# Kernel optimization log

Hardware: AMD Instinct MI355X
Metric: run time of the kernel (lower is better)

## Reference

```python
import jax, jax.numpy as jnp
import numpy as np

B, S, E, H, A, C = 128, 1024, 2048, 300, 5, 3


def setup_inputs() -> dict:
    key = jax.random.key(0)
    ks = jax.random.split(key, 14)
    sc = 0.05
    return {
        "h": jax.random.normal(ks[0], (B, S, H), jnp.float32),
        "edge_index": jax.random.randint(ks[1], (B, 2, E), 0, S, dtype=jnp.int32),
        "edge_weight": jax.random.uniform(ks[2], (B, E), jnp.float32),
        "aspect_pos": jax.random.randint(ks[3], (B, A), 0, S, dtype=jnp.int32),
        "W_span": jax.random.normal(ks[4], (H, H), jnp.float32) * sc,
        "b_span": jnp.zeros((H,), jnp.float32),
        "W1": jax.random.normal(ks[5], (H, H), jnp.float32) * sc,
        "b1": jnp.zeros((H,), jnp.float32),
        "W2": jax.random.normal(ks[6], (H, H), jnp.float32) * sc,
        "b2": jnp.zeros((H,), jnp.float32),
        "W_gate": jax.random.normal(ks[7], (2 * H, H), jnp.float32) * sc,
        "b_gate": jnp.zeros((H,), jnp.float32),
        "W_cls": jax.random.normal(ks[8], (H, C), jnp.float32) * sc,
        "b_cls": jnp.zeros((C,), jnp.float32),
    }


def _gcn_conv(x, src, dst, ew, W, b):
    # PyG GCNConv: xW, add self-loops (w=1), symmetric norm, scatter-sum at dst.
    n = x.shape[0]
    xw = x @ W  # [S, H]
    deg = jnp.zeros((n,), x.dtype).at[dst].add(ew) + 1.0  # +1 from self-loop
    dinv = jax.lax.rsqrt(deg)
    norm = dinv[src] * ew * dinv[dst]  # [E]
    msg = norm[:, None] * xw[src]  # [E, H]
    out = jax.ops.segment_sum(msg, dst, num_segments=n)
    out = out + xw / deg[:, None]  # self-loop: dinv[i]^2 * xw[i]
    return out + b


def reference(h, edge_index, edge_weight, aspect_pos,
              W_span, b_span, W1, b1, W2, b2, W_gate, b_gate, W_cls, b_cls):
    def per_sample(h_i, ei, ew, ap):
        # aspect-attention span pooling
        aspect_vec = h_i[ap].mean(0)  # [H]
        q = aspect_vec @ W_span + b_span
        attn = jax.nn.softmax(h_i @ q)  # [S]
        span = attn @ h_i  # [H]
        # 2-layer GCN over dependency edges
        src, dst = ei[0], ei[1]
        x = jax.nn.relu(_gcn_conv(h_i, src, dst, ew, W1, b1))
        x = _gcn_conv(x, src, dst, ew, W2, b2)
        syn = x[ap].mean(0)  # [H]
        return span, syn

    span, syn = jax.vmap(per_sample)(h, edge_index, edge_weight, aspect_pos)
    gate = jax.nn.sigmoid(jnp.concatenate([span, syn], axis=-1) @ W_gate + b_gate)
    fused = gate * syn + (1.0 - gate) * span
    return fused @ W_cls + b_cls  # [B, C]
```

## Files before the change

kernel.cpp:

```cpp
#include <hip/hip_runtime.h>
#include <math.h>

#define BB 128
#define SS 1024
#define EE 2048
#define HH 300
#define AA 5
#define CC 3
#define NB 8
#define PSTRIDE 304
#define EMAX 2049


__global__ void k_init(float* deg, float* syn) {
    int gid = blockIdx.x * blockDim.x + threadIdx.x;
    if (gid < BB * SS) deg[gid] = 1.0f;
    if (gid < BB * HH) syn[gid] = 0.0f;
}

__global__ void k_deg(const int* __restrict__ eidx, const float* __restrict__ ew,
                      float* __restrict__ deg) {
    int gid = blockIdx.x * blockDim.x + threadIdx.x;
    if (gid >= BB * EE) return;
    int b = gid >> 11;
    int e = gid & (EE - 1);
    int d = eidx[(size_t)b * 2 * EE + EE + e];
    atomicAdd(&deg[b * SS + d], ew[(size_t)b * EE + e]);
}

__global__ __launch_bounds__(320) void k_q(const float* __restrict__ h, const int* __restrict__ ap,
                                           const float* __restrict__ W_span, const float* __restrict__ b_span,
                                           float* __restrict__ qbuf) {
    int b = blockIdx.x;
    __shared__ float av[HH];
    const float* hb = h + (size_t)b * SS * HH;
    for (int j = threadIdx.x; j < HH; j += blockDim.x) {
        float s = 0.f;
        for (int a = 0; a < AA; ++a) s += hb[(size_t)ap[b * AA + a] * HH + j];
        av[j] = s * (1.0f / AA);
    }
    __syncthreads();
    for (int j = threadIdx.x; j < HH; j += blockDim.x) {
        float acc = b_span[j];
        for (int i = 0; i < HH; ++i) acc += av[i] * W_span[i * HH + j];
        qbuf[b * HH + j] = acc;
    }
}

__global__ __launch_bounds__(256) void k_span_part(const float* __restrict__ h,
                                                   const float* __restrict__ qbuf,
                                                   float* __restrict__ part) {
    int b = blockIdx.x / NB, nb = blockIdx.x % NB;
    int tid = threadIdx.x, lane = tid & 63, w = tid >> 6;
    const float* hb = h + (size_t)b * SS * HH;
    const float* qb = qbuf + b * HH;
    float qr[5];
#pragma unroll
    for (int k = 0; k < 5; ++k) { int idx = lane + 64 * k; qr[k] = (idx < HH) ? qb[idx] : 0.f; }
    float m = -INFINITY, l = 0.f;
    float acc[5] = {0.f, 0.f, 0.f, 0.f, 0.f};
    int row0 = nb * (SS / NB) + w * 32;
    for (int t = 0; t < 32; ++t) {
        const float* hr = hb + (size_t)(row0 + t) * HH;
        float hv[5]; float pd = 0.f;
#pragma unroll
        for (int k = 0; k < 5; ++k) {
            int idx = lane + 64 * k;
            hv[k] = (idx < HH) ? hr[idx] : 0.f;
            pd += hv[k] * qr[k];
        }
#pragma unroll
        for (int off = 32; off > 0; off >>= 1) pd += __shfl_xor(pd, off, 64);
        float mn = fmaxf(m, pd);
        float sc = __expf(m - mn);
        float p  = __expf(pd - mn);
        l = l * sc + p;
#pragma unroll
        for (int k = 0; k < 5; ++k) acc[k] = acc[k] * sc + p * hv[k];
        m = mn;
    }
    __shared__ float sm[4], sl[4], sacc[4][PSTRIDE];
#pragma unroll
    for (int k = 0; k < 5; ++k) { int idx = lane + 64 * k; if (idx < HH) sacc[w][idx] = acc[k]; }
    if (lane == 0) { sm[w] = m; sl[w] = l; }
    __syncthreads();
    float M = fmaxf(fmaxf(sm[0], sm[1]), fmaxf(sm[2], sm[3]));
    float* pb = part + ((size_t)b * NB + nb) * PSTRIDE;
    for (int j = tid; j < HH; j += 256) {
        float s = 0.f;
#pragma unroll
        for (int ww = 0; ww < 4; ++ww) s += sacc[ww][j] * __expf(sm[ww] - M);
        pb[j] = s;
    }
    if (tid == 0) {
        float L = 0.f;
        for (int ww = 0; ww < 4; ++ww) L += sl[ww] * __expf(sm[ww] - M);
        pb[300] = L; pb[301] = M;
    }
}

__global__ __launch_bounds__(256) void k_span_final(const float* __restrict__ part,
                                                    float* __restrict__ span) {
    int b = blockIdx.x; int tid = threadIdx.x;
    const float* pb = part + (size_t)b * NB * PSTRIDE;
    float M = -INFINITY;
    for (int nb = 0; nb < NB; ++nb) M = fmaxf(M, pb[nb * PSTRIDE + 301]);
    float L = 0.f;
    for (int nb = 0; nb < NB; ++nb) L += pb[nb * PSTRIDE + 300] * __expf(pb[nb * PSTRIDE + 301] - M);
    float invL = 1.0f / L;
    for (int j = tid; j < HH; j += blockDim.x) {
        float s = 0.f;
        for (int nb = 0; nb < NB; ++nb) s += pb[nb * PSTRIDE + j] * __expf(pb[nb * PSTRIDE + 301] - M);
        span[b * HH + j] = s * invL;
    }
}

__global__ __launch_bounds__(320) void k_syn(const float* __restrict__ h, const int* __restrict__ eidx,
                                             const float* __restrict__ ew, const int* __restrict__ ap,
                                             const float* __restrict__ W1, const float* __restrict__ b1,
                                             const float* __restrict__ W2, const float* __restrict__ b2,
                                             const float* __restrict__ deg, float* __restrict__ syn) {
    int b = blockIdx.x / AA, a = blockIdx.x % AA;
    int tid = threadIdx.x;
    const int* srcA = eidx + (size_t)b * 2 * EE;
    const int* dstA = srcA + EE;
    const float* ewb  = ew + (size_t)b * EE;
    const float* hb   = h + (size_t)b * SS * HH;
    const float* degb = deg + (size_t)b * SS;
    __shared__ float z[HH], svec[HH];
    __shared__ float lco_c[EMAX]; __shared__ int lco_r[EMAX];
    __shared__ float lci_c[EMAX]; __shared__ int lci_r[EMAX];
    __shared__ int lco_cnt, lci_cnt;

    int pos = ap[b * AA + a];
    for (int j = tid; j < HH; j += blockDim.x) z[j] = 0.f;
    if (tid == 0) { lco_cnt = 1; lco_c[0] = 1.0f / degb[pos]; lco_r[0] = pos; }
    __syncthreads();
    float dip = rsqrtf(degb[pos]);
    for (int e = tid; e < EE; e += blockDim.x) {
        if (dstA[e] == pos) {
            int k = atomicAdd(&lco_cnt, 1);
            if (k < EMAX) { lco_c[k] = rsqrtf(degb[srcA[e]]) * ewb[e] * dip; lco_r[k] = srcA[e]; }
        }
    }
    __syncthreads();
    int nc = lco_cnt; if (nc > EMAX) nc = EMAX;

    for (int ci = 0; ci < nc; ++ci) {
        int r = lco_r[ci]; float cr = lco_c[ci];
        if (tid == 0) { lci_cnt = 1; lci_c[0] = 1.0f / degb[r]; lci_r[0] = r; }
        __syncthreads();
        float dir = rsqrtf(degb[r]);
        for (int e = tid; e < EE; e += blockDim.x) {
            if (dstA[e] == r) {
                int k = atomicAdd(&lci_cnt, 1);
                if (k < EMAX) { lci_c[k] = rsqrtf(degb[srcA[e]]) * ewb[e] * dir; lci_r[k] = srcA[e]; }
            }
        }
        __syncthreads();
        int ni = lci_cnt; if (ni > EMAX) ni = EMAX;
        for (int j = tid; j < HH; j += blockDim.x) {
            float s = 0.f;
            for (int k = 0; k < ni; ++k) s += lci_c[k] * hb[(size_t)lci_r[k] * HH + j];
            svec[j] = s;
        }
        __syncthreads();
        for (int j = tid; j < HH; j += blockDim.x) {
            float acc2 = b1[j];
            for (int i = 0; i < HH; ++i) acc2 += svec[i] * W1[i * HH + j];
            z[j] += cr * fmaxf(acc2, 0.f);
        }
        __syncthreads();
    }
    for (int j = tid; j < HH; j += blockDim.x) {
        float acc2 = b2[j];
        for (int i = 0; i < HH; ++i) acc2 += z[i] * W2[i * HH + j];
        atomicAdd(&syn[b * HH + j], acc2 * (1.0f / AA));
    }
}

__global__ __launch_bounds__(320) void k_head(const float* __restrict__ span, const float* __restrict__ syn,
                                              const float* __restrict__ W_gate, const float* __restrict__ b_gate,
                                              const float* __restrict__ W_cls, const float* __restrict__ b_cls,
                                              float* __restrict__ out) {
    int b = blockIdx.x; int tid = threadIdx.x;
    __shared__ float ssp[HH], ssy[HH], outc[CC];
    for (int j = tid; j < HH; j += blockDim.x) { ssp[j] = span[b * HH + j]; ssy[j] = syn[b * HH + j]; }
    if (tid < CC) outc[tid] = 0.f;
    __syncthreads();
    for (int j = tid; j < HH; j += blockDim.x) {
        float acc = b_gate[j];
        for (int i = 0; i < HH; ++i)
            acc += ssp[i] * W_gate[i * HH + j] + ssy[i] * W_gate[(HH + i) * HH + j];
        float g = 1.0f / (1.0f + __expf(-acc));
        float f = g * ssy[j] + (1.0f - g) * ssp[j];
        for (int c = 0; c < CC; ++c) atomicAdd(&outc[c], f * W_cls[j * CC + c]);
    }
    __syncthreads();
    if (tid < CC) out[b * CC + tid] = b_cls[tid] + outc[tid];
}

extern "C" void kernel_launch(void* const* d_in, const int* in_sizes, int n_in,
                              void* d_out, int out_size, void* d_ws, size_t ws_size,
                              hipStream_t stream) {
    const float* h      = (const float*)d_in[0];
    const int*   eidx   = (const int*)d_in[1];
    const float* ew     = (const float*)d_in[2];
    const int*   ap     = (const int*)d_in[3];
    const float* W_span = (const float*)d_in[4];
    const float* b_span = (const float*)d_in[5];
    const float* W1     = (const float*)d_in[6];
    const float* b1     = (const float*)d_in[7];
    const float* W2     = (const float*)d_in[8];
    const float* b2     = (const float*)d_in[9];
    const float* W_gate = (const float*)d_in[10];
    const float* b_gate = (const float*)d_in[11];
    const float* W_cls  = (const float*)d_in[12];
    const float* b_cls  = (const float*)d_in[13];
    float* out = (float*)d_out;

    float* w    = (float*)d_ws;
    float* deg  = w;
    float* qbuf = deg + BB * SS;
    float* part = qbuf + BB * HH;
    float* span = part + BB * NB * PSTRIDE;
    float* syn  = span + BB * HH;

    hipLaunchKernelGGL(k_init, dim3((BB * SS + 255) / 256), dim3(256), 0, stream, deg, syn);
    hipLaunchKernelGGL(k_deg, dim3((BB * EE + 255) / 256), dim3(256), 0, stream, eidx, ew, deg);
    hipLaunchKernelGGL(k_q, dim3(BB), dim3(320), 0, stream, h, ap, W_span, b_span, qbuf);
    hipLaunchKernelGGL(k_span_part, dim3(BB * NB), dim3(256), 0, stream, h, qbuf, part);
    hipLaunchKernelGGL(k_span_final, dim3(BB), dim3(256), 0, stream, part, span);
    hipLaunchKernelGGL(k_syn, dim3(BB * AA), dim3(320), 0, stream, h, eidx, ew, ap, W1, b1, W2, b2, deg, syn);
    hipLaunchKernelGGL(k_head, dim3(BB), dim3(320), 0, stream, span, syn, W_gate, b_gate, W_cls, b_cls, out);
}
```

Baseline: 408.7 us.

## Restructure GCN syntactic path: dedupe neighbors, chunked edge scans, warp-split matvecs

Rewrites the per-aspect two-hop GCN computation. Neighbor coefficients are accumulated per node so duplicates merge, and neighbors are processed in chunks of 16 with a single edge scan per chunk that uses wave ballots and shared atomics. The W2 projection is hoisted out of the per-aspect blocks into a separate per-sample kernel after summing z across aspects. All the 300x300 matvecs (q, W1, W2, gate) are split across the five waves with partial sums, which replaces serial per-thread loops and the shared-atomic classifier reduction. This adds shared-atomic contention and an extra kernel launch.

```diff
diff --git a/kernel.cpp b/kernel.cpp
--- a/kernel.cpp
+++ b/kernel.cpp
@@ -9,13 +9,13 @@
 #define CC 3
 #define NB 8
 #define PSTRIDE 304
-#define EMAX 2049
-
-
-__global__ void k_init(float* deg, float* syn) {
+#define CH 16
+
+
+__global__ void k_init(float* deg, float* zbuf) {
     int gid = blockIdx.x * blockDim.x + threadIdx.x;
     if (gid < BB * SS) deg[gid] = 1.0f;
-    if (gid < BB * HH) syn[gid] = 0.0f;
+    if (gid < BB * HH) zbuf[gid] = 0.0f;
 }
 
 __global__ void k_deg(const int* __restrict__ eidx, const float* __restrict__ ew,
@@ -32,19 +32,29 @@
                                            const float* __restrict__ W_span, const float* __restrict__ b_span,
                                            float* __restrict__ qbuf) {
     int b = blockIdx.x;
+    int tid = threadIdx.x, lane = tid & 63, w = tid >> 6;
     __shared__ float av[HH];
+    __shared__ float psum[5][PSTRIDE];
     const float* hb = h + (size_t)b * SS * HH;
-    for (int j = threadIdx.x; j < HH; j += blockDim.x) {
+    for (int j = tid; j < HH; j += 320) {
         float s = 0.f;
         for (int a = 0; a < AA; ++a) s += hb[(size_t)ap[b * AA + a] * HH + j];
         av[j] = s * (1.0f / AA);
     }
     __syncthreads();
-    for (int j = threadIdx.x; j < HH; j += blockDim.x) {
-        float acc = b_span[j];
-        for (int i = 0; i < HH; ++i) acc += av[i] * W_span[i * HH + j];
-        qbuf[b * HH + j] = acc;
-    }
+    float acc[5] = {0.f, 0.f, 0.f, 0.f, 0.f};
+    for (int ii = 0; ii < 60; ++ii) {
+        int i = w * 60 + ii;
+        float sv = av[i];
+        const float* wr = W_span + (size_t)i * HH;
+#pragma unroll
+        for (int k = 0; k < 5; ++k) { int j = lane + 64 * k; if (j < HH) acc[k] = fmaf(sv, wr[j], acc[k]); }
+    }
+#pragma unroll
+    for (int k = 0; k < 5; ++k) { int j = lane + 64 * k; if (j < HH) psum[w][j] = acc[k]; }
+    __syncthreads();
+    for (int j = tid; j < HH; j += 320)
+        qbuf[b * HH + j] = b_span[j] + psum[0][j] + psum[1][j] + psum[2][j] + psum[3][j] + psum[4][j];
 }
 
 __global__ __launch_bounds__(256) void k_span_part(const float* __restrict__ h,
@@ -115,89 +125,173 @@
     }
 }
 
-__global__ __launch_bounds__(320) void k_syn(const float* __restrict__ h, const int* __restrict__ eidx,
-                                             const float* __restrict__ ew, const int* __restrict__ ap,
-                                             const float* __restrict__ W1, const float* __restrict__ b1,
-                                             const float* __restrict__ W2, const float* __restrict__ b2,
-                                             const float* __restrict__ deg, float* __restrict__ syn) {
+__global__ __launch_bounds__(320) void k_syn1(const float* __restrict__ h, const int* __restrict__ eidx,
+                                              const float* __restrict__ ew, const int* __restrict__ ap,
+                                              const float* __restrict__ W1, const float* __restrict__ b1,
+                                              const float* __restrict__ deg, float* __restrict__ zbuf) {
     int b = blockIdx.x / AA, a = blockIdx.x % AA;
-    int tid = threadIdx.x;
+    int tid = threadIdx.x, lane = tid & 63, w = tid >> 6;
     const int* srcA = eidx + (size_t)b * 2 * EE;
     const int* dstA = srcA + EE;
     const float* ewb  = ew + (size_t)b * EE;
     const float* hb   = h + (size_t)b * SS * HH;
     const float* degb = deg + (size_t)b * SS;
-    __shared__ float z[HH], svec[HH];
-    __shared__ float lco_c[EMAX]; __shared__ int lco_r[EMAX];
-    __shared__ float lci_c[EMAX]; __shared__ int lci_r[EMAX];
-    __shared__ int lco_cnt, lci_cnt;
+
+    __shared__ float wv[SS];
+    __shared__ int   idxmap[SS];
+    __shared__ int   rl[SS];
+    __shared__ float cf[SS];
+    __shared__ float U[CH][HH];
+    __shared__ float psum[5][PSTRIDE];
+    __shared__ float z[HH];
+    __shared__ int   cnt;
 
     int pos = ap[b * AA + a];
-    for (int j = tid; j < HH; j += blockDim.x) z[j] = 0.f;
-    if (tid == 0) { lco_cnt = 1; lco_c[0] = 1.0f / degb[pos]; lco_r[0] = pos; }
-    __syncthreads();
+    for (int r = tid; r < SS; r += 320) wv[r] = 0.f;
+    for (int j = tid; j < HH; j += 320) z[j] = 0.f;
+    if (tid == 0) cnt = 0;
+    __syncthreads();
+
     float dip = rsqrtf(degb[pos]);
-    for (int e = tid; e < EE; e += blockDim.x) {
-        if (dstA[e] == pos) {
-            int k = atomicAdd(&lco_cnt, 1);
-            if (k < EMAX) { lco_c[k] = rsqrtf(degb[srcA[e]]) * ewb[e] * dip; lco_r[k] = srcA[e]; }
+    if (tid == 0) atomicAdd(&wv[pos], 1.0f / degb[pos]);
+    for (int e = tid; e < EE; e += 320) {
+        if (dstA[e] == pos)
+            atomicAdd(&wv[srcA[e]], rsqrtf(degb[srcA[e]]) * ewb[e] * dip);
+    }
+    __syncthreads();
+
+    for (int r = tid; r < SS; r += 320) {
+        float c = wv[r];
+        if (c > 0.f) { int k = atomicAdd(&cnt, 1); rl[k] = r; cf[k] = c; }
+    }
+    __syncthreads();
+    int nc = cnt;
+
+    for (int c0 = 0; c0 < nc; c0 += CH) {
+        int ch = min(CH, nc - c0);
+        for (int r = tid; r < SS; r += 320) idxmap[r] = -1;
+        __syncthreads();
+        if (tid < ch) idxmap[rl[c0 + tid]] = tid;
+        __syncthreads();
+        for (int t = 0; t < ch; ++t) {
+            int r = rl[c0 + t]; float sc = 1.0f / degb[r];
+            const float* hr = hb + (size_t)r * HH;
+            for (int j = tid; j < HH; j += 320) U[t][j] = hr[j] * sc;
         }
-    }
-    __syncthreads();
-    int nc = lco_cnt; if (nc > EMAX) nc = EMAX;
-
-    for (int ci = 0; ci < nc; ++ci) {
-        int r = lco_r[ci]; float cr = lco_c[ci];
-        if (tid == 0) { lci_cnt = 1; lci_c[0] = 1.0f / degb[r]; lci_r[0] = r; }
         __syncthreads();
-        float dir = rsqrtf(degb[r]);
-        for (int e = tid; e < EE; e += blockDim.x) {
-            if (dstA[e] == r) {
-                int k = atomicAdd(&lci_cnt, 1);
-                if (k < EMAX) { lci_c[k] = rsqrtf(degb[srcA[e]]) * ewb[e] * dir; lci_r[k] = srcA[e]; }
+        for (int e0 = 0; e0 < EE; e0 += 320) {
+            int e = e0 + tid;
+            bool hit = false; int t = -1, s = 0; float co = 0.f;
+            if (e < EE) {
+                int d = dstA[e];
+                t = idxmap[d];
+                if (t >= 0) {
+                    s = srcA[e];
+                    co = rsqrtf(degb[s]) * ewb[e] * rsqrtf(degb[d]);
+                    hit = true;
+                }
+            }
+            unsigned long long mask = __ballot(hit);
+            while (mask) {
+                int l = __ffsll((unsigned long long)mask) - 1; mask &= mask - 1;
+                int ts = __shfl(t, l); int ss = __shfl(s, l); float cs = __shfl(co, l);
+                const float* hr = hb + (size_t)ss * HH;
+#pragma unroll
+                for (int k = 0; k < 5; ++k) { int j = lane + 64 * k; if (j < HH) atomicAdd(&U[ts][j], cs * hr[j]); }
             }
         }
         __syncthreads();
-        int ni = lci_cnt; if (ni > EMAX) ni = EMAX;
-        for (int j = tid; j < HH; j += blockDim.x) {
-            float s = 0.f;
-            for (int k = 0; k < ni; ++k) s += lci_c[k] * hb[(size_t)lci_r[k] * HH + j];
-            svec[j] = s;
+        for (int t = 0; t < ch; ++t) {
+            float acc[5] = {0.f, 0.f, 0.f, 0.f, 0.f};
+            for (int ii = 0; ii < 60; ++ii) {
+                int i = w * 60 + ii;
+                float sv = U[t][i];
+                const float* wr = W1 + (size_t)i * HH;
+#pragma unroll
+                for (int k = 0; k < 5; ++k) { int j = lane + 64 * k; if (j < HH) acc[k] = fmaf(sv, wr[j], acc[k]); }
+            }
+#pragma unroll
+            for (int k = 0; k < 5; ++k) { int j = lane + 64 * k; if (j < HH) psum[w][j] = acc[k]; }
+            __syncthreads();
+            float cr = cf[c0 + t];
+            for (int j = tid; j < HH; j += 320) {
+                float v = b1[j] + psum[0][j] + psum[1][j] + psum[2][j] + psum[3][j] + psum[4][j];
+                z[j] += cr * fmaxf(v, 0.f);
+            }
+            __syncthreads();
         }
-        __syncthreads();
-        for (int j = tid; j < HH; j += blockDim.x) {
-            float acc2 = b1[j];
-            for (int i = 0; i < HH; ++i) acc2 += svec[i] * W1[i * HH + j];
-            z[j] += cr * fmaxf(acc2, 0.f);
-        }
-        __syncthreads();
-    }
-    for (int j = tid; j < HH; j += blockDim.x) {
-        float acc2 = b2[j];
-        for (int i = 0; i < HH; ++i) acc2 += z[i] * W2[i * HH + j];
-        atomicAdd(&syn[b * HH + j], acc2 * (1.0f / AA));
-    }
+    }
+    for (int j = tid; j < HH; j += 320) atomicAdd(&zbuf[b * HH + j], z[j]);
+}
+
+__global__ __launch_bounds__(320) void k_syn2(const float* __restrict__ zbuf,
+                                              const float* __restrict__ W2, const float* __restrict__ b2,
+                                              float* __restrict__ syn) {
+    int b = blockIdx.x;
+    int tid = threadIdx.x, lane = tid & 63, w = tid >> 6;
+    __shared__ float zl[HH];
+    __shared__ float psum[5][PSTRIDE];
+    for (int j = tid; j < HH; j += 320) zl[j] = zbuf[b * HH + j];
+    __syncthreads();
+    float acc[5] = {0.f, 0.f, 0.f, 0.f, 0.f};
+    for (int ii = 0; ii < 60; ++ii) {
+        int i = w * 60 + ii;
+        float sv = zl[i];
+        const float* wr = W2 + (size_t)i * HH;
+#pragma unroll
+        for (int k = 0; k < 5; ++k) { int j = lane + 64 * k; if (j < HH) acc[k] = fmaf(sv, wr[j], acc[k]); }
+    }
+#pragma unroll
+    for (int k = 0; k < 5; ++k) { int j = lane + 64 * k; if (j < HH) psum[w][j] = acc[k]; }
+    __syncthreads();
+    for (int j = tid; j < HH; j += 320)
+        syn[b * HH + j] = b2[j] + (psum[0][j] + psum[1][j] + psum[2][j] + psum[3][j] + psum[4][j]) * (1.0f / AA);
 }
 
 __global__ __launch_bounds__(320) void k_head(const float* __restrict__ span, const float* __restrict__ syn,
                                               const float* __restrict__ W_gate, const float* __restrict__ b_gate,
                                               const float* __restrict__ W_cls, const float* __restrict__ b_cls,
                                               float* __restrict__ out) {
-    int b = blockIdx.x; int tid = threadIdx.x;
-    __shared__ float ssp[HH], ssy[HH], outc[CC];
-    for (int j = tid; j < HH; j += blockDim.x) { ssp[j] = span[b * HH + j]; ssy[j] = syn[b * HH + j]; }
-    if (tid < CC) outc[tid] = 0.f;
-    __syncthreads();
-    for (int j = tid; j < HH; j += blockDim.x) {
-        float acc = b_gate[j];
-        for (int i = 0; i < HH; ++i)
-            acc += ssp[i] * W_gate[i * HH + j] + ssy[i] * W_gate[(HH + i) * HH + j];
-        float g = 1.0f / (1.0f + __expf(-acc));
+    int b = blockIdx.x;
+    int tid = threadIdx.x, lane = tid & 63, w = tid >> 6;
+    __shared__ float ssp[HH], ssy[HH];
+    __shared__ float psum[5][PSTRIDE];
+    __shared__ float csum[5][CC];
+    for (int j = tid; j < HH; j += 320) { ssp[j] = span[b * HH + j]; ssy[j] = syn[b * HH + j]; }
+    __syncthreads();
+    float acc[5] = {0.f, 0.f, 0.f, 0.f, 0.f};
+    for (int ii = 0; ii < 120; ++ii) {
+        int i = w * 120 + ii;
+        float sv = (i < HH) ? ssp[i] : ssy[i - HH];
+        const float* wr = W_gate + (size_t)i * HH;
+#pragma unroll
+        for (int k = 0; k < 5; ++k) { int j = lane + 64 * k; if (j < HH) acc[k] = fmaf(sv, wr[j], acc[k]); }
+    }
+#pragma unroll
+    for (int k = 0; k < 5; ++k) { int j = lane + 64 * k; if (j < HH) psum[w][j] = acc[k]; }
+    __syncthreads();
+    float c0 = 0.f, c1 = 0.f, c2 = 0.f;
+    int j = tid;
+    if (j < HH) {
+        float g = 1.0f / (1.0f + __expf(-(b_gate[j] + psum[0][j] + psum[1][j] + psum[2][j] + psum[3][j] + psum[4][j])));
         float f = g * ssy[j] + (1.0f - g) * ssp[j];
-        for (int c = 0; c < CC; ++c) atomicAdd(&outc[c], f * W_cls[j * CC + c]);
-    }
-    __syncthreads();
-    if (tid < CC) out[b * CC + tid] = b_cls[tid] + outc[tid];
+        c0 = f * W_cls[j * CC + 0];
+        c1 = f * W_cls[j * CC + 1];
+        c2 = f * W_cls[j * CC + 2];
+    }
+#pragma unroll
+    for (int off = 32; off > 0; off >>= 1) {
+        c0 += __shfl_xor(c0, off, 64);
+        c1 += __shfl_xor(c1, off, 64);
+        c2 += __shfl_xor(c2, off, 64);
+    }
+    if (lane == 0) { csum[w][0] = c0; csum[w][1] = c1; csum[w][2] = c2; }
+    __syncthreads();
+    if (tid < CC) {
+        float s = b_cls[tid];
+        for (int ww = 0; ww < 5; ++ww) s += csum[ww][tid];
+        out[b * CC + tid] = s;
+    }
 }
 
 extern "C" void kernel_launch(void* const* d_in, const int* in_sizes, int n_in,
@@ -224,13 +318,15 @@
     float* qbuf = deg + BB * SS;
     float* part = qbuf + BB * HH;
     float* span = part + BB * NB * PSTRIDE;
-    float* syn  = span + BB * HH;
-
-    hipLaunchKernelGGL(k_init, dim3((BB * SS + 255) / 256), dim3(256), 0, stream, deg, syn);
+    float* zbuf = span + BB * HH;
+    float* syn  = zbuf + BB * HH;
+
+    hipLaunchKernelGGL(k_init, dim3(512), dim3(256), 0, stream, deg, zbuf);
     hipLaunchKernelGGL(k_deg, dim3((BB * EE + 255) / 256), dim3(256), 0, stream, eidx, ew, deg);
     hipLaunchKernelGGL(k_q, dim3(BB), dim3(320), 0, stream, h, ap, W_span, b_span, qbuf);
     hipLaunchKernelGGL(k_span_part, dim3(BB * NB), dim3(256), 0, stream, h, qbuf, part);
     hipLaunchKernelGGL(k_span_final, dim3(BB), dim3(256), 0, stream, part, span);
-    hipLaunchKernelGGL(k_syn, dim3(BB * AA), dim3(320), 0, stream, h, eidx, ew, ap, W1, b1, W2, b2, deg, syn);
+    hipLaunchKernelGGL(k_syn1, dim3(BB * AA), dim3(320), 0, stream, h, eidx, ew, ap, W1, b1, deg, zbuf);
+    hipLaunchKernelGGL(k_syn2, dim3(BB), dim3(320), 0, stream, zbuf, W2, b2, syn);
     hipLaunchKernelGGL(k_head, dim3(BB), dim3(320), 0, stream, span, syn, W_gate, b_gate, W_cls, b_cls, out);
 }
```

After: 605.4 us. +48.1%, slower.
